# Performance work log

Hardware: AMD Instinct MI355X
Metric: run time of the kernel (lower is better)

The kernel has to match this reference:

```python
import jax, jax.numpy as jnp
import numpy as np

OUT, IN, GS = 8192, 8192, 128
N_GROUPS = OUT * IN // GS  # 524288


def setup_inputs() -> dict:
    key = jax.random.key(0)
    k1, k2, k3 = jax.random.split(key, 3)
    x = jax.random.normal(k1, (32, IN), dtype=jnp.float32)
    # ternary values in {-1, 0, 1}
    ternary = jax.random.randint(k2, (OUT, IN), -1, 2, dtype=jnp.int32)
    # positive per-group scales
    scales = jax.random.uniform(k3, (N_GROUPS,), dtype=jnp.float32, minval=0.01, maxval=0.1)
    return {"x": x, "ternary": ternary, "scales": scales}


def reference(x, ternary, scales):
    # Dequantize: each contiguous group of GS weights shares one scale.
    # scales: [n_groups] -> [n_groups, GS] -> [OUT, IN]
    scales_exp = jnp.broadcast_to(scales[:, None], (N_GROUPS, GS)).reshape(OUT, IN)
    w = ternary.astype(jnp.float32) * scales_exp  # [OUT, IN]
    # F.linear(x, w) = x @ w.T
    return jnp.einsum("ti,oi->to", x, w)
```

## Files before the change

kernel.cpp:

```cpp
#include <hip/hip_runtime.h>
#include <hip/hip_bf16.h>
#include <stdint.h>

#define OUT_DIM 8192
#define IN_DIM  8192
#define GS      128
#define MROWS   32

typedef __attribute__((ext_vector_type(8))) short bf16x8;
typedef __attribute__((ext_vector_type(4))) float f32x4;
typedef __attribute__((ext_vector_type(8))) unsigned short u16x8;

__device__ __forceinline__ unsigned short f2bf_rne(float f) {
    uint32_t v = __builtin_bit_cast(uint32_t, f);
    v += 0x7FFFu + ((v >> 16) & 1u);
    return (unsigned short)(v >> 16);
}

__global__ __launch_bounds__(256) void prep_xbf(const float* __restrict__ x,
                                                unsigned short* __restrict__ xbf) {
    int i = (blockIdx.x * 256 + threadIdx.x) * 8;
    float4 a = *(const float4*)(x + i);
    float4 b = *(const float4*)(x + i + 4);
    float f[8] = {a.x, a.y, a.z, a.w, b.x, b.y, b.z, b.w};
    u16x8 u;
#pragma unroll
    for (int j = 0; j < 8; ++j) u[j] = f2bf_rne(f[j]);
    *(u16x8*)(xbf + i) = u;
}

template <bool USE_WS>
__global__ __launch_bounds__(256, 4) void ternary_gemm(
    const int* __restrict__ tern, const float* __restrict__ scales,
    const float* __restrict__ xf, const unsigned short* __restrict__ xbf,
    float* __restrict__ out) {
    const int wave = blockIdx.x * 4 + (threadIdx.x >> 6);
    const int lane = threadIdx.x & 63;
    const int kc    = wave >> 9;
    const int ntile = wave & 511;
    const int n    = lane & 15;
    const int quad = lane >> 4;
    const int o      = (ntile << 4) + n;
    const int k0base = kc << 10;

    const int* __restrict__ wrow = tern + (size_t)o * IN_DIM;
    const int r0 = n, r1 = 16 + n;

    f32x4 acc0 = {0.f, 0.f, 0.f, 0.f};
    f32x4 acc1 = {0.f, 0.f, 0.f, 0.f};

    for (int it = 0; it < 8; ++it) {
        const int k0 = k0base + (it << 7);
        const unsigned short sb = f2bf_rne(scales[o * (IN_DIM / GS) + (k0 >> 7)]);
        const unsigned int pos = sb, neg = sb | 0x8000u;
#pragma unroll
        for (int st = 0; st < 4; ++st) {
            const int k = k0 + (st << 5) + (quad << 3);
            int4 w0 = *(const int4*)(wrow + k);
            int4 w1 = *(const int4*)(wrow + k + 4);
            int tw[8] = {w0.x, w0.y, w0.z, w0.w, w1.x, w1.y, w1.z, w1.w};
            bf16x8 bfr;
#pragma unroll
            for (int j = 0; j < 8; ++j) {
                int t = tw[j];
                unsigned int u = (t < 0) ? neg : pos;
                bfr[j] = (short)((t == 0) ? 0u : u);
            }
            bf16x8 a0, a1;
            if constexpr (USE_WS) {
                a0 = *(const bf16x8*)(xbf + r0 * IN_DIM + k);
                a1 = *(const bf16x8*)(xbf + r1 * IN_DIM + k);
            } else {
                float4 xa = *(const float4*)(xf + r0 * IN_DIM + k);
                float4 xb = *(const float4*)(xf + r0 * IN_DIM + k + 4);
                float4 xc = *(const float4*)(xf + r1 * IN_DIM + k);
                float4 xd = *(const float4*)(xf + r1 * IN_DIM + k + 4);
                float fa[8] = {xa.x, xa.y, xa.z, xa.w, xb.x, xb.y, xb.z, xb.w};
                float fb[8] = {xc.x, xc.y, xc.z, xc.w, xd.x, xd.y, xd.z, xd.w};
#pragma unroll
                for (int j = 0; j < 8; ++j) { a0[j] = (short)f2bf_rne(fa[j]); a1[j] = (short)f2bf_rne(fb[j]); }
            }
            acc0 = __builtin_amdgcn_mfma_f32_16x16x32_bf16(a0, bfr, acc0, 0, 0, 0);
            acc1 = __builtin_amdgcn_mfma_f32_16x16x32_bf16(a1, bfr, acc1, 0, 0, 0);
        }
    }

#pragma unroll
    for (int r = 0; r < 4; ++r) {
        const int t = quad * 4 + r;
        unsafeAtomicAdd(out + (size_t)t * OUT_DIM + o, acc0[r]);
        unsafeAtomicAdd(out + (size_t)(t + 16) * OUT_DIM + o, acc1[r]);
    }
}

extern "C" void kernel_launch(void* const* d_in, const int* in_sizes, int n_in,
                              void* d_out, int out_size, void* d_ws, size_t ws_size,
                              hipStream_t stream) {
    const float* x      = (const float*)d_in[0];
    const int*   tern   = (const int*)d_in[1];
    const float* scales = (const float*)d_in[2];
    float* out = (float*)d_out;
    unsigned short* xbf = (unsigned short*)d_ws;

    const bool use_ws = ws_size >= (size_t)MROWS * IN_DIM * sizeof(unsigned short);

    hipMemsetAsync(d_out, 0, (size_t)out_size * sizeof(float), stream);
    if (use_ws) {
        prep_xbf<<<(MROWS * IN_DIM) / (256 * 8), 256, 0, stream>>>(x, xbf);
        ternary_gemm<true><<<1024, 256, 0, stream>>>(tern, scales, x, xbf, out);
    } else {
        ternary_gemm<false><<<1024, 256, 0, stream>>>(tern, scales, x, xbf, out);
    }
}
```

Measured before the change: 394.4 us.

## Replace atomic split-K accumulation with partial buffers and a reduction kernel

Each K-chunk wave now writes its partial sums to its own slice of a workspace buffer instead of issuing atomic adds into the output, and a separate kernel sums the eight partials. This drops the output memset and the atomic traffic. It also prefetches the next group scale ahead of use and builds the signed bf16 weight with a bitwise OR of the sign bit rather than a select. The cost is an extra kernel launch and about 8 MB of partial writes and reads, and it assumes the workspace is large enough with no fallback path.

```diff
diff --git a/kernel.cpp b/kernel.cpp
--- a/kernel.cpp
+++ b/kernel.cpp
@@ -6,6 +6,8 @@
 #define IN_DIM  8192
 #define GS      128
 #define MROWS   32
+#define NSPLIT  8
+#define PART_ELEMS (MROWS * OUT_DIM)
 
 typedef __attribute__((ext_vector_type(8))) short bf16x8;
 typedef __attribute__((ext_vector_type(4))) float f32x4;
@@ -29,68 +31,71 @@
     *(u16x8*)(xbf + i) = u;
 }
 
-template <bool USE_WS>
 __global__ __launch_bounds__(256, 4) void ternary_gemm(
     const int* __restrict__ tern, const float* __restrict__ scales,
-    const float* __restrict__ xf, const unsigned short* __restrict__ xbf,
-    float* __restrict__ out) {
-    const int wave = blockIdx.x * 4 + (threadIdx.x >> 6);
-    const int lane = threadIdx.x & 63;
+    const unsigned short* __restrict__ xbf, float* __restrict__ part) {
+    const int wave  = blockIdx.x * 4 + (threadIdx.x >> 6);
+    const int lane  = threadIdx.x & 63;
     const int kc    = wave >> 9;
     const int ntile = wave & 511;
-    const int n    = lane & 15;
-    const int quad = lane >> 4;
+    const int n     = lane & 15;
+    const int quad  = lane >> 4;
     const int o      = (ntile << 4) + n;
     const int k0base = kc << 10;
 
     const int* __restrict__ wrow = tern + (size_t)o * IN_DIM;
-    const int r0 = n, r1 = 16 + n;
+    const unsigned short* __restrict__ xr0 = xbf + n * IN_DIM;
+    const unsigned short* __restrict__ xr1 = xbf + (16 + n) * IN_DIM;
+
+    const float* __restrict__ sp = scales + o * (IN_DIM / GS) + (kc << 3);
+    float s_cur = sp[0];
 
     f32x4 acc0 = {0.f, 0.f, 0.f, 0.f};
     f32x4 acc1 = {0.f, 0.f, 0.f, 0.f};
 
     for (int it = 0; it < 8; ++it) {
+        const unsigned int p = f2bf_rne(s_cur);
+        float s_nxt = sp[(it < 7) ? (it + 1) : 7];
         const int k0 = k0base + (it << 7);
-        const unsigned short sb = f2bf_rne(scales[o * (IN_DIM / GS) + (k0 >> 7)]);
-        const unsigned int pos = sb, neg = sb | 0x8000u;
 #pragma unroll
         for (int st = 0; st < 4; ++st) {
             const int k = k0 + (st << 5) + (quad << 3);
             int4 w0 = *(const int4*)(wrow + k);
             int4 w1 = *(const int4*)(wrow + k + 4);
+            bf16x8 a0 = *(const bf16x8*)(xr0 + k);
+            bf16x8 a1 = *(const bf16x8*)(xr1 + k);
             int tw[8] = {w0.x, w0.y, w0.z, w0.w, w1.x, w1.y, w1.z, w1.w};
             bf16x8 bfr;
 #pragma unroll
             for (int j = 0; j < 8; ++j) {
                 int t = tw[j];
-                unsigned int u = (t < 0) ? neg : pos;
-                bfr[j] = (short)((t == 0) ? 0u : u);
-            }
-            bf16x8 a0, a1;
-            if constexpr (USE_WS) {
-                a0 = *(const bf16x8*)(xbf + r0 * IN_DIM + k);
-                a1 = *(const bf16x8*)(xbf + r1 * IN_DIM + k);
-            } else {
-                float4 xa = *(const float4*)(xf + r0 * IN_DIM + k);
-                float4 xb = *(const float4*)(xf + r0 * IN_DIM + k + 4);
-                float4 xc = *(const float4*)(xf + r1 * IN_DIM + k);
-                float4 xd = *(const float4*)(xf + r1 * IN_DIM + k + 4);
-                float fa[8] = {xa.x, xa.y, xa.z, xa.w, xb.x, xb.y, xb.z, xb.w};
-                float fb[8] = {xc.x, xc.y, xc.z, xc.w, xd.x, xd.y, xd.z, xd.w};
-#pragma unroll
-                for (int j = 0; j < 8; ++j) { a0[j] = (short)f2bf_rne(fa[j]); a1[j] = (short)f2bf_rne(fb[j]); }
+                unsigned int v = p | ((unsigned int)t & 0x8000u);
+                bfr[j] = (short)((t == 0) ? 0u : v);
             }
             acc0 = __builtin_amdgcn_mfma_f32_16x16x32_bf16(a0, bfr, acc0, 0, 0, 0);
             acc1 = __builtin_amdgcn_mfma_f32_16x16x32_bf16(a1, bfr, acc1, 0, 0, 0);
         }
+        s_cur = s_nxt;
     }
 
+    float* __restrict__ prow = part + (size_t)kc * PART_ELEMS;
 #pragma unroll
     for (int r = 0; r < 4; ++r) {
-        const int t = quad * 4 + r;
-        unsafeAtomicAdd(out + (size_t)t * OUT_DIM + o, acc0[r]);
-        unsafeAtomicAdd(out + (size_t)(t + 16) * OUT_DIM + o, acc1[r]);
+        prow[(quad * 4 + r) * OUT_DIM + o]        = acc0[r];
+        prow[(quad * 4 + r + 16) * OUT_DIM + o]   = acc1[r];
     }
+}
+
+__global__ __launch_bounds__(256) void reduce_parts(const float* __restrict__ part,
+                                                    float* __restrict__ out) {
+    const int i = (blockIdx.x * 256 + threadIdx.x) * 4;
+    float4 s = *(const float4*)(part + i);
+#pragma unroll
+    for (int kc = 1; kc < NSPLIT; ++kc) {
+        float4 v = *(const float4*)(part + (size_t)kc * PART_ELEMS + i);
+        s.x += v.x; s.y += v.y; s.z += v.z; s.w += v.w;
+    }
+    *(float4*)(out + i) = s;
 }
 
 extern "C" void kernel_launch(void* const* d_in, const int* in_sizes, int n_in,
@@ -100,15 +105,11 @@
     const int*   tern   = (const int*)d_in[1];
     const float* scales = (const float*)d_in[2];
     float* out = (float*)d_out;
+
     unsigned short* xbf = (unsigned short*)d_ws;
+    float* part = (float*)((char*)d_ws + (512 << 10));
 
-    const bool use_ws = ws_size >= (size_t)MROWS * IN_DIM * sizeof(unsigned short);
-
-    hipMemsetAsync(d_out, 0, (size_t)out_size * sizeof(float), stream);
-    if (use_ws) {
-        prep_xbf<<<(MROWS * IN_DIM) / (256 * 8), 256, 0, stream>>>(x, xbf);
-        ternary_gemm<true><<<1024, 256, 0, stream>>>(tern, scales, x, xbf, out);
-    } else {
-        ternary_gemm<false><<<1024, 256, 0, stream>>>(tern, scales, x, xbf, out);
-    }
+    prep_xbf<<<128, 256, 0, stream>>>(x, xbf);
+    ternary_gemm<<<1024, 256, 0, stream>>>(tern, scales, xbf, part);
+    reduce_parts<<<256, 256, 0, stream>>>(part, out);
 }
```

Result: slower. 406.7 us (+3.1%).
